# Optimization experiments

Hardware: AMD Instinct MI355X
Metric: run time of the kernel (lower is better)

The kernel has to match this reference:

```python
import jax, jax.numpy as jnp
import numpy as np


def setup_inputs() -> dict:
    key = jax.random.key(0)
    ks = jax.random.split(key, 12)
    N, E, D_IN, D_H, R, B, G, C, D_E = 50000, 600000, 128, 128, 8, 4, 64, 16, 16
    x = jax.random.normal(ks[0], (N, D_IN), dtype=jnp.float32)
    edge_index = jax.random.randint(ks[1], (2, E), 0, N, dtype=jnp.int64)
    edge_type = jax.random.randint(ks[2], (E,), 0, R, dtype=jnp.int64)
    edge_attr = jax.random.normal(ks[3], (E, D_E), dtype=jnp.float32)
    batch = jnp.sort(jax.random.randint(ks[4], (N,), 0, G, dtype=jnp.int64))
    # RGCNConv basis-decomposition params + root + bias
    basis = jax.random.normal(ks[5], (B, D_IN, D_H), dtype=jnp.float32) / np.sqrt(D_IN)
    comp = jax.random.normal(ks[6], (R, B), dtype=jnp.float32) / np.sqrt(B)
    root = jax.random.normal(ks[7], (D_IN, D_H), dtype=jnp.float32) / np.sqrt(D_IN)
    bias = jnp.zeros((D_H,), dtype=jnp.float32)
    fc_w = jax.random.normal(ks[8], (D_H, C), dtype=jnp.float32) / np.sqrt(D_H)
    fc_b = jnp.zeros((C,), dtype=jnp.float32)
    return {"x": x, "edge_index": edge_index, "edge_type": edge_type,
            "edge_attr": edge_attr, "batch": batch, "num_graphs": 64,
            "basis": basis, "comp": comp, "root": root, "bias": bias,
            "fc_w": fc_w, "fc_b": fc_b}


def reference(x, edge_index, edge_type, edge_attr, batch, num_graphs,
              basis, comp, root, bias, fc_w, fc_b):
    N = x.shape[0]
    R = comp.shape[0]
    src, dst = edge_index[0], edge_index[1]
    # relation weights from basis decomposition: [R, in, out]
    W = jnp.einsum('rb,bio->rio', comp, basis)
    x_src = x[src]  # gather source features [E, in]
    agg = jnp.zeros((N, W.shape[2]), dtype=x.dtype)
    # per-relation mean aggregation (PyG RGCNConv default), summed over relations
    for r in range(R):
        mask = (edge_type == r).astype(x.dtype)  # [E]
        msg = (x_src @ W[r]) * mask[:, None]     # [E, out]
        summed = jax.ops.segment_sum(msg, dst, num_segments=N)
        cnt = jax.ops.segment_sum(mask, dst, num_segments=N)
        agg = agg + summed / jnp.maximum(cnt, 1.0)[:, None]
    h = jax.nn.relu(x @ root + bias + agg)       # [N, hidden]
    # global mean pool over graphs
    pooled_sum = jax.ops.segment_sum(h, batch, num_segments=num_graphs)
    gcnt = jax.ops.segment_sum(jnp.ones((N,), dtype=x.dtype), batch, num_segments=num_graphs)
    pooled = pooled_sum / jnp.maximum(gcnt, 1.0)[:, None]  # [G, hidden]
    return pooled @ fc_w + fc_b                  # [G, num_classes]
```

## Files before the change

kernel.cpp:

```cpp
#include <hip/hip_runtime.h>

static inline int ceil_div(int a, int b){ return (a+b-1)/b; }
static inline size_t align_up(size_t x, size_t a){ return (x + a - 1) / a * a; }

typedef __bf16 bf16x8 __attribute__((ext_vector_type(8)));
typedef float  f32x4  __attribute__((ext_vector_type(4)));

static __device__ inline unsigned short f2bf(float f){
    unsigned int u = __float_as_uint(f);
    unsigned int lsb = (u >> 16) & 1u;
    u += 0x7FFFu + lsb;
    return (unsigned short)(u >> 16);
}
static __device__ inline float bf2f(unsigned short b){
    return __uint_as_float(((unsigned int)b) << 16);
}
static __device__ inline unsigned int packbf(float a, float b){
    return (unsigned int)f2bf(a) | ((unsigned int)f2bf(b) << 16);
}

static __device__ inline void gload_lds16(const void* g, void* l) {
    __builtin_amdgcn_global_load_lds(
        (const __attribute__((address_space(1))) unsigned int*)g,
        (__attribute__((address_space(3))) unsigned int*)l, 16, 0, 0);
}

__global__ void compute_Bt_kernel(const float* __restrict__ comp, const float* __restrict__ basis,
                                  const float* __restrict__ root, unsigned short* __restrict__ Bt,
                                  int B) {
    int idx = blockIdx.x*blockDim.x + threadIdx.x;
    if (idx >= 128*1152) return;
    int o = idx / 1152, kk = idx - o*1152;
    float val;
    if (kk < 1024) {
        int r = kk >> 7, i = kk & 127;
        val = 0.f;
        for (int b = 0; b < B; ++b)
            val += comp[r*B+b] * basis[((size_t)b*128 + i)*128 + o];
    } else {
        val = root[(size_t)(kk-1024)*128 + o];
    }
    Bt[idx] = f2bf(val);
}

__global__ void count_kernel(const int* __restrict__ dst, const int* __restrict__ et,
                             int* __restrict__ cnt, int E, int R) {
    int e = blockIdx.x*blockDim.x + threadIdx.x;
    if (e >= E) return;
    atomicAdd(&cnt[(size_t)dst[e]*R + et[e]], 1);
}

__global__ __launch_bounds__(256)
void scan_block_kernel(const int* __restrict__ in, int* __restrict__ out,
                       int* __restrict__ bsums, int n) {
    __shared__ int tsum[256];
    int t = threadIdx.x;
    int idx0 = blockIdx.x*1024 + t*4;
    int v0 = (idx0+0 < n) ? in[idx0+0] : 0;
    int v1 = (idx0+1 < n) ? in[idx0+1] : 0;
    int v2 = (idx0+2 < n) ? in[idx0+2] : 0;
    int v3 = (idx0+3 < n) ? in[idx0+3] : 0;
    int s = v0+v1+v2+v3;
    tsum[t] = s; __syncthreads();
    for (int off = 1; off < 256; off <<= 1) {
        int x = (t >= off) ? tsum[t-off] : 0;
        __syncthreads();
        tsum[t] += x;
        __syncthreads();
    }
    int run = tsum[t] - s;
    if (idx0+0 < n) out[idx0+0] = run; run += v0;
    if (idx0+1 < n) out[idx0+1] = run; run += v1;
    if (idx0+2 < n) out[idx0+2] = run; run += v2;
    if (idx0+3 < n) out[idx0+3] = run;
    if (bsums && t == 255) bsums[blockIdx.x] = tsum[255];
}

__global__ void scan_add_kernel(int* __restrict__ out, const int* __restrict__ bs,
                                int n, int total) {
    int i = blockIdx.x*blockDim.x + threadIdx.x;
    if (i < n) out[i] += bs[i >> 10];
    if (i == 0) out[n] = total;
}

__global__ void fill_kernel(const int* __restrict__ src, const int* __restrict__ dst,
                            const int* __restrict__ et, int* __restrict__ offsets,
                            int* __restrict__ slot_src, int E, int R) {
    int e = blockIdx.x*blockDim.x + threadIdx.x;
    if (e >= E) return;
    int bin = dst[e]*R + et[e];
    int slot = atomicAdd(&offsets[bin], 1);
    slot_src[slot] = src[e];
}

__global__ __launch_bounds__(256)
void xb_kernel(const float* __restrict__ x, unsigned int* __restrict__ Xb2, int N) {
    int t = blockIdx.x*blockDim.x + threadIdx.x;
    int n = t >> 6;
    if (n >= N) return;
    int l = t & 63;
    float2 v = reinterpret_cast<const float2*>(x + (size_t)n*128)[l];
    Xb2[(size_t)n*64 + l] = packbf(v.x, v.y);
}

__global__ __launch_bounds__(256)
void aggregate_kernel(const int* __restrict__ offsets, const int* __restrict__ slot_src,
                      const unsigned int* __restrict__ Xb2, unsigned int* __restrict__ Mc2,
                      int N) {
    int gw = (int)((blockIdx.x*blockDim.x + threadIdx.x) >> 6);
    int node = gw >> 2, part = gw & 3;
    if (node >= N) return;
    int l = threadIdx.x & 63;
    int base = node*8 + part*2;
    int lo   = (base == 0) ? 0 : offsets[base-1];
    int bmid = offsets[base];
    int hi   = offsets[base+1];

    float ax0=0.f, ay0=0.f, ax1=0.f, ay1=0.f;

#define ACC2(E_, U_) { \
    float vx_ = bf2f((unsigned short)((U_) & 0xFFFFu)); \
    float vy_ = bf2f((unsigned short)((U_) >> 16)); \
    if ((E_) < bmid) { ax0 += vx_; ay0 += vy_; } \
    else             { ax1 += vx_; ay1 += vy_; } }

    for (int e = lo; e < hi; e += 4) {
        int hm = hi - 1;
        int i1 = (e+1 < hm) ? e+1 : hm;
        int i2 = (e+2 < hm) ? e+2 : hm;
        int i3 = (e+3 < hm) ? e+3 : hm;
        int s0 = slot_src[e];
        int s1 = slot_src[i1];
        int s2 = slot_src[i2];
        int s3 = slot_src[i3];
        unsigned int u0 = Xb2[(size_t)s0*64 + l];
        unsigned int u1 = Xb2[(size_t)s1*64 + l];
        unsigned int u2 = Xb2[(size_t)s2*64 + l];
        unsigned int u3 = Xb2[(size_t)s3*64 + l];
        if (e+1 >= hi) u1 = 0u;
        if (e+2 >= hi) u2 = 0u;
        if (e+3 >= hi) u3 = 0u;
        ACC2(e+0, u0) ACC2(e+1, u1) ACC2(e+2, u2) ACC2(e+3, u3)
    }
#undef ACC2

    unsigned int* Mrow = Mc2 + (size_t)node*512;
    float i0 = 1.f/fmaxf((float)(bmid-lo), 1.f);
    float i1 = 1.f/fmaxf((float)(hi-bmid), 1.f);
    __builtin_nontemporal_store(packbf(ax0*i0, ay0*i0), &Mrow[(2*part+0)*64 + l]);
    __builtin_nontemporal_store(packbf(ax1*i1, ay1*i1), &Mrow[(2*part+1)*64 + l]);
}

__global__ __launch_bounds__(256)
void mfma_gemm_kernel(const unsigned short* __restrict__ Mc,
                      const unsigned short* __restrict__ Xb,
                      const unsigned short* __restrict__ Btc,
                      const float* __restrict__ bias,
                      unsigned short* __restrict__ h) {
    __shared__ char ldsA[64*128];
    __shared__ char ldsB[128*128];

    int tid  = threadIdx.x;
    int lane = tid & 63;
    int wid  = tid >> 6;
    int rg = wid & 1, cg = wid >> 1;
    int fr = lane & 15, kb = lane >> 4;
    long m0 = (long)blockIdx.x * 64;

    int lrow8 = lane >> 3;
    int lcb   = (lane & 7) * 16;

    f32x4 acc[2][4];
    #pragma unroll
    for (int mf = 0; mf < 2; ++mf)
        #pragma unroll
        for (int nf = 0; nf < 4; ++nf) acc[mf][nf] = f32x4{0.f,0.f,0.f,0.f};

    const char* McB = (const char*)Mc;
    const char* XbB = (const char*)Xb;
    const char* BtB = (const char*)Btc;

    for (int t = 0; t < 18; ++t) {
        #pragma unroll
        for (int i = 0; i < 2; ++i) {
            int row = wid*16 + i*8 + lrow8;
            int sw  = lcb ^ ((row & 7) << 4);
            const char* g = (t < 16)
                ? McB + (size_t)(m0 + row)*2048 + t*128 + sw
                : XbB + (size_t)(m0 + row)*256 + (t-16)*128 + sw;
            gload_lds16(g, &ldsA[wid*2048 + i*1024 + lane*16]);
        }
        #pragma unroll
        for (int i = 0; i < 4; ++i) {
            int col = wid*32 + i*8 + lrow8;
            int sw  = lcb ^ ((col & 7) << 4);
            const char* g = BtB + (size_t)col*2304 + t*128 + sw;
            gload_lds16(g, &ldsB[wid*4096 + i*1024 + lane*16]);
        }
        __syncthreads();

        bf16x8 af[2][2], bf[4][2];
        #pragma unroll
        for (int mf = 0; mf < 2; ++mf) {
            int row = rg*32 + mf*16 + fr;
            #pragma unroll
            for (int kk = 0; kk < 2; ++kk) {
                int byte = row*128 + ((kk*64 + kb*16) ^ ((row & 7) << 4));
                af[mf][kk] = *reinterpret_cast<const bf16x8*>(&ldsA[byte]);
            }
        }
        #pragma unroll
        for (int nf = 0; nf < 4; ++nf) {
            int col = cg*64 + nf*16 + fr;
            #pragma unroll
            for (int kk = 0; kk < 2; ++kk) {
                int byte = col*128 + ((kk*64 + kb*16) ^ ((col & 7) << 4));
                bf[nf][kk] = *reinterpret_cast<const bf16x8*>(&ldsB[byte]);
            }
        }
        #pragma unroll
        for (int kk = 0; kk < 2; ++kk)
            #pragma unroll
            for (int mf = 0; mf < 2; ++mf)
                #pragma unroll
                for (int nf = 0; nf < 4; ++nf)
                    acc[mf][nf] = __builtin_amdgcn_mfma_f32_16x16x32_bf16(
                        af[mf][kk], bf[nf][kk], acc[mf][nf], 0, 0, 0);
        __syncthreads();
    }

    float bb[4];
    #pragma unroll
    for (int nf = 0; nf < 4; ++nf) bb[nf] = bias[cg*64 + nf*16 + fr];

    #pragma unroll
    for (int mf = 0; mf < 2; ++mf)
        #pragma unroll
        for (int q = 0; q < 4; ++q) {
            long r = m0 + rg*32 + mf*16 + kb*4 + q;
            unsigned short* hr = h + (size_t)r*128 + cg*64;
            #pragma unroll
            for (int nf = 0; nf < 4; ++nf)
                hr[nf*16 + fr] = f2bf(fmaxf(acc[mf][nf][q] + bb[nf], 0.f));
        }
}

__global__ __launch_bounds__(512)
void pool_fc_kernel(const unsigned int* __restrict__ h2, const int* __restrict__ batch,
                    const float* __restrict__ fw, const float* __restrict__ fb,
                    float* __restrict__ out, int N, int C) {
    int g = blockIdx.x;
    int t = threadIdx.x;
    int lo = 0, hi = N;
    while (lo < hi) { int mid = (lo+hi) >> 1; if (batch[mid] < g) lo = mid+1; else hi = mid; }
    int s0 = lo;
    hi = N;
    while (lo < hi) { int mid = (lo+hi) >> 1; if (batch[mid] < g+1) lo = mid+1; else hi = mid; }
    int s1 = lo;

    int d2 = t & 63;
    float ax = 0.f, ay = 0.f;
    for (int row = s0 + (t >> 6); row < s1; row += 8) {
        unsigned int u = h2[(size_t)row*64 + d2];
        ax += bf2f((unsigned short)(u & 0xFFFFu));
        ay += bf2f((unsigned short)(u >> 16));
    }
    __shared__ float ps[128];
    if (t < 128) ps[t] = 0.f;
    __syncthreads();
    atomicAdd(&ps[2*d2],   ax);
    atomicAdd(&ps[2*d2+1], ay);
    __syncthreads();
    if (t < C) {
        float inv = 1.f / fmaxf((float)(s1 - s0), 1.f);
        float s = 0.f;
        #pragma unroll 4
        for (int k = 0; k < 128; ++k) s += ps[k] * fw[(size_t)k*C + t];
        out[(size_t)g*C + t] = s * inv + fb[t];
    }
}

extern "C" void kernel_launch(void* const* d_in, const int* in_sizes, int n_in,
                              void* d_out, int out_size, void* d_ws, size_t ws_size,
                              hipStream_t stream) {
    const float* x       = (const float*)d_in[0];
    const int*   eindex  = (const int*)  d_in[1];
    const int*   etype   = (const int*)  d_in[2];
    const int*   batch   = (const int*)  d_in[4];
    const float* basis   = (const float*)d_in[6];
    const float* comp    = (const float*)d_in[7];
    const float* root    = (const float*)d_in[8];
    const float* bias    = (const float*)d_in[9];
    const float* fc_w    = (const float*)d_in[10];
    const float* fc_b    = (const float*)d_in[11];

    int N  = in_sizes[4];
    int E  = in_sizes[2];
    int C  = in_sizes[11];
    int G  = out_size / C;
    int IO = in_sizes[8];
    int B  = in_sizes[6] / IO;
    int R  = in_sizes[7] / B;
    int NR = N * R;
    int MB = ceil_div(N, 64);
    int Mpad = MB * 64;

    const int* src = eindex;
    const int* dst = eindex + E;

    char* base = (char*)d_ws;
    size_t off = 0;
    auto alloc = [&](size_t bytes) -> char* {
        char* p = base + off;
        off = align_up(off + bytes, 256);
        return p;
    };
    unsigned short* Bt  = (unsigned short*)alloc(sizeof(unsigned short)*128*1152);
    int*   cnt      = (int*)  alloc(sizeof(int)*(size_t)NR);
    int*   offsets  = (int*)  alloc(sizeof(int)*((size_t)NR+1));
    int*   bsums    = (int*)  alloc(sizeof(int)*1024);
    int*   slot_src = (int*)  alloc(sizeof(int)*(size_t)E);
    unsigned short* h  = (unsigned short*)alloc(sizeof(unsigned short)*(size_t)Mpad*128);
    unsigned short* Xb = (unsigned short*)alloc(sizeof(unsigned short)*(size_t)Mpad*128);
    unsigned short* Mc = (unsigned short*)alloc(sizeof(unsigned short)*(size_t)Mpad*1024);

    hipMemsetAsync(cnt, 0, sizeof(int)*(size_t)NR, stream);
    compute_Bt_kernel<<<ceil_div(128*1152,256),256,0,stream>>>(comp, basis, root, Bt, B);
    count_kernel<<<ceil_div(E,256),256,0,stream>>>(dst, etype, cnt, E, R);

    int nb = ceil_div(NR, 1024);
    scan_block_kernel<<<nb,256,0,stream>>>(cnt, offsets, bsums, NR);
    scan_block_kernel<<<1,256,0,stream>>>(bsums, bsums, nullptr, nb);
    scan_add_kernel<<<ceil_div(NR,256),256,0,stream>>>(offsets, bsums, NR, E);

    fill_kernel<<<ceil_div(E,256),256,0,stream>>>(src, dst, etype, offsets, slot_src, E, R);

    xb_kernel<<<ceil_div(N*64,256),256,0,stream>>>(x, (unsigned int*)Xb, N);
    aggregate_kernel<<<ceil_div(N*4*64,256),256,0,stream>>>(offsets, slot_src,
                                                            (const unsigned int*)Xb,
                                                            (unsigned int*)Mc, N);

    mfma_gemm_kernel<<<MB,256,0,stream>>>(Mc, Xb, Bt, bias, h);

    pool_fc_kernel<<<G,512,0,stream>>>((const unsigned int*)h, batch, fc_w, fc_b,
                                       (float*)d_out, N, C);
}
```

Measured before the change: 220.1 us.

## Split GEMM output columns across blocks, parallelize pooling, pad edge slots

The GEMM now gives each block a 64-row by 64-column output tile, so there are twice as many blocks, ordered so that eight row blocks share each column half. This raises occupancy on the 50k-row problem. Pooling is spread over 8 chunks per graph with global float atomics into a zeroed psum buffer, and a separate small FC kernel finishes the result. The slot_src array gains four zero pad entries, which removes the clamped index math in the aggregate loop. The costs are reading each A tile twice, the extra FC launch, and atomic contention.

After: 217.4 us. About the same (-1.2%).

```diff
diff --git a/kernel.cpp b/kernel.cpp
--- a/kernel.cpp
+++ b/kernel.cpp
@@ -88,6 +88,7 @@
                             int* __restrict__ slot_src, int E, int R) {
     int e = blockIdx.x*blockDim.x + threadIdx.x;
     if (e >= E) return;
+    if (e < 4) slot_src[E + e] = 0;
     int bin = dst[e]*R + et[e];
     int slot = atomicAdd(&offsets[bin], 1);
     slot_src[slot] = src[e];
@@ -125,14 +126,10 @@
     else             { ax1 += vx_; ay1 += vy_; } }
 
     for (int e = lo; e < hi; e += 4) {
-        int hm = hi - 1;
-        int i1 = (e+1 < hm) ? e+1 : hm;
-        int i2 = (e+2 < hm) ? e+2 : hm;
-        int i3 = (e+3 < hm) ? e+3 : hm;
         int s0 = slot_src[e];
-        int s1 = slot_src[i1];
-        int s2 = slot_src[i2];
-        int s3 = slot_src[i3];
+        int s1 = slot_src[e+1];
+        int s2 = slot_src[e+2];
+        int s3 = slot_src[e+3];
         unsigned int u0 = Xb2[(size_t)s0*64 + l];
         unsigned int u1 = Xb2[(size_t)s1*64 + l];
         unsigned int u2 = Xb2[(size_t)s2*64 + l];
@@ -156,25 +153,31 @@
                       const unsigned short* __restrict__ Xb,
                       const unsigned short* __restrict__ Btc,
                       const float* __restrict__ bias,
-                      unsigned short* __restrict__ h) {
+                      unsigned short* __restrict__ h, int MBrows) {
     __shared__ char ldsA[64*128];
-    __shared__ char ldsB[128*128];
+    __shared__ char ldsB[64*128];
 
     int tid  = threadIdx.x;
     int lane = tid & 63;
     int wid  = tid >> 6;
     int rg = wid & 1, cg = wid >> 1;
     int fr = lane & 15, kb = lane >> 4;
-    long m0 = (long)blockIdx.x * 64;
+
+    int blk = blockIdx.x;
+    int q = blk >> 4, rem = blk & 15, c = rem >> 3, m = rem & 7;
+    int rb = q*8 + m;
+    if (rb >= MBrows) return;
+    long m0 = (long)rb * 64;
+    int colbase = c * 64;
 
     int lrow8 = lane >> 3;
     int lcb   = (lane & 7) * 16;
 
-    f32x4 acc[2][4];
+    f32x4 acc[2][2];
     #pragma unroll
     for (int mf = 0; mf < 2; ++mf)
         #pragma unroll
-        for (int nf = 0; nf < 4; ++nf) acc[mf][nf] = f32x4{0.f,0.f,0.f,0.f};
+        for (int nf = 0; nf < 2; ++nf) acc[mf][nf] = f32x4{0.f,0.f,0.f,0.f};
 
     const char* McB = (const char*)Mc;
     const char* XbB = (const char*)Xb;
@@ -191,15 +194,15 @@
             gload_lds16(g, &ldsA[wid*2048 + i*1024 + lane*16]);
         }
         #pragma unroll
-        for (int i = 0; i < 4; ++i) {
-            int col = wid*32 + i*8 + lrow8;
+        for (int i = 0; i < 2; ++i) {
+            int col = wid*16 + i*8 + lrow8;
             int sw  = lcb ^ ((col & 7) << 4);
-            const char* g = BtB + (size_t)col*2304 + t*128 + sw;
-            gload_lds16(g, &ldsB[wid*4096 + i*1024 + lane*16]);
+            const char* g = BtB + (size_t)(colbase + col)*2304 + t*128 + sw;
+            gload_lds16(g, &ldsB[wid*2048 + i*1024 + lane*16]);
         }
         __syncthreads();
 
-        bf16x8 af[2][2], bf[4][2];
+        bf16x8 af[2][2], bfr[2][2];
         #pragma unroll
         for (int mf = 0; mf < 2; ++mf) {
             int row = rg*32 + mf*16 + fr;
@@ -210,12 +213,12 @@
             }
         }
         #pragma unroll
-        for (int nf = 0; nf < 4; ++nf) {
-            int col = cg*64 + nf*16 + fr;
+        for (int nf = 0; nf < 2; ++nf) {
+            int col = cg*32 + nf*16 + fr;
             #pragma unroll
             for (int kk = 0; kk < 2; ++kk) {
                 int byte = col*128 + ((kk*64 + kb*16) ^ ((col & 7) << 4));
-                bf[nf][kk] = *reinterpret_cast<const bf16x8*>(&ldsB[byte]);
+                bfr[nf][kk] = *reinterpret_cast<const bf16x8*>(&ldsB[byte]);
             }
         }
         #pragma unroll
@@ -223,32 +226,31 @@
             #pragma unroll
             for (int mf = 0; mf < 2; ++mf)
                 #pragma unroll
-                for (int nf = 0; nf < 4; ++nf)
+                for (int nf = 0; nf < 2; ++nf)
                     acc[mf][nf] = __builtin_amdgcn_mfma_f32_16x16x32_bf16(
-                        af[mf][kk], bf[nf][kk], acc[mf][nf], 0, 0, 0);
+                        af[mf][kk], bfr[nf][kk], acc[mf][nf], 0, 0, 0);
         __syncthreads();
     }
 
-    float bb[4];
+    float bb[2];
     #pragma unroll
-    for (int nf = 0; nf < 4; ++nf) bb[nf] = bias[cg*64 + nf*16 + fr];
+    for (int nf = 0; nf < 2; ++nf) bb[nf] = bias[colbase + cg*32 + nf*16 + fr];
 
     #pragma unroll
     for (int mf = 0; mf < 2; ++mf)
         #pragma unroll
-        for (int q = 0; q < 4; ++q) {
-            long r = m0 + rg*32 + mf*16 + kb*4 + q;
-            unsigned short* hr = h + (size_t)r*128 + cg*64;
+        for (int q2 = 0; q2 < 4; ++q2) {
+            long r = m0 + rg*32 + mf*16 + kb*4 + q2;
+            unsigned short* hr = h + (size_t)r*128 + colbase + cg*32;
             #pragma unroll
-            for (int nf = 0; nf < 4; ++nf)
-                hr[nf*16 + fr] = f2bf(fmaxf(acc[mf][nf][q] + bb[nf], 0.f));
-        }
-}
-
-__global__ __launch_bounds__(512)
-void pool_fc_kernel(const unsigned int* __restrict__ h2, const int* __restrict__ batch,
-                    const float* __restrict__ fw, const float* __restrict__ fb,
-                    float* __restrict__ out, int N, int C) {
+            for (int nf = 0; nf < 2; ++nf)
+                hr[nf*16 + fr] = f2bf(fmaxf(acc[mf][nf][q2] + bb[nf], 0.f));
+        }
+}
+
+__global__ __launch_bounds__(256)
+void pool_kernel(const unsigned int* __restrict__ h2, const int* __restrict__ batch,
+                 float* __restrict__ psum, int N) {
     int g = blockIdx.x;
     int t = threadIdx.x;
     int lo = 0, hi = N;
@@ -257,27 +259,39 @@
     hi = N;
     while (lo < hi) { int mid = (lo+hi) >> 1; if (batch[mid] < g+1) lo = mid+1; else hi = mid; }
     int s1 = lo;
+    int len = s1 - s0;
+    int chunk = blockIdx.y, NC = gridDim.y;
+    int a = s0 + (int)((long long)len * chunk / NC);
+    int b = s0 + (int)((long long)len * (chunk+1) / NC);
 
     int d2 = t & 63;
     float ax = 0.f, ay = 0.f;
-    for (int row = s0 + (t >> 6); row < s1; row += 8) {
+    for (int row = a + (t >> 6); row < b; row += 4) {
         unsigned int u = h2[(size_t)row*64 + d2];
         ax += bf2f((unsigned short)(u & 0xFFFFu));
         ay += bf2f((unsigned short)(u >> 16));
     }
-    __shared__ float ps[128];
-    if (t < 128) ps[t] = 0.f;
-    __syncthreads();
-    atomicAdd(&ps[2*d2],   ax);
-    atomicAdd(&ps[2*d2+1], ay);
-    __syncthreads();
-    if (t < C) {
-        float inv = 1.f / fmaxf((float)(s1 - s0), 1.f);
-        float s = 0.f;
-        #pragma unroll 4
-        for (int k = 0; k < 128; ++k) s += ps[k] * fw[(size_t)k*C + t];
-        out[(size_t)g*C + t] = s * inv + fb[t];
-    }
+    atomicAdd(&psum[(size_t)g*128 + 2*d2    ], ax);
+    atomicAdd(&psum[(size_t)g*128 + 2*d2 + 1], ay);
+}
+
+__global__ void fc_kernel(const float* __restrict__ psum, const int* __restrict__ batch,
+                          const float* __restrict__ fw, const float* __restrict__ fb,
+                          float* __restrict__ out, int N, int G, int C) {
+    int idx = blockIdx.x*blockDim.x + threadIdx.x;
+    if (idx >= G*C) return;
+    int g = idx / C, cc = idx - g*C;
+    int lo = 0, hi = N;
+    while (lo < hi) { int mid = (lo+hi) >> 1; if (batch[mid] < g) lo = mid+1; else hi = mid; }
+    int s0 = lo;
+    hi = N;
+    while (lo < hi) { int mid = (lo+hi) >> 1; if (batch[mid] < g+1) lo = mid+1; else hi = mid; }
+    float inv = 1.f / fmaxf((float)(lo - s0), 1.f);
+    float s = fb[cc];
+    #pragma unroll 4
+    for (int k = 0; k < 128; ++k)
+        s += psum[(size_t)g*128 + k] * inv * fw[(size_t)k*C + cc];
+    out[idx] = s;
 }
 
 extern "C" void kernel_launch(void* const* d_in, const int* in_sizes, int n_in,
@@ -304,6 +318,7 @@
     int NR = N * R;
     int MB = ceil_div(N, 64);
     int Mpad = MB * 64;
+    int grid_gemm = ceil_div(MB, 8) * 16;
 
     const int* src = eindex;
     const int* dst = eindex + E;
@@ -317,14 +332,15 @@
     };
     unsigned short* Bt  = (unsigned short*)alloc(sizeof(unsigned short)*128*1152);
     int*   cnt      = (int*)  alloc(sizeof(int)*(size_t)NR);
+    float* psum     = (float*)alloc(sizeof(float)*(size_t)G*128);
     int*   offsets  = (int*)  alloc(sizeof(int)*((size_t)NR+1));
     int*   bsums    = (int*)  alloc(sizeof(int)*1024);
-    int*   slot_src = (int*)  alloc(sizeof(int)*(size_t)E);
+    int*   slot_src = (int*)  alloc(sizeof(int)*((size_t)E+4));
     unsigned short* h  = (unsigned short*)alloc(sizeof(unsigned short)*(size_t)Mpad*128);
     unsigned short* Xb = (unsigned short*)alloc(sizeof(unsigned short)*(size_t)Mpad*128);
     unsigned short* Mc = (unsigned short*)alloc(sizeof(unsigned short)*(size_t)Mpad*1024);
 
-    hipMemsetAsync(cnt, 0, sizeof(int)*(size_t)NR, stream);
+    hipMemsetAsync(cnt, 0, (size_t)((char*)(psum + (size_t)G*128) - (char*)cnt), stream);
     compute_Bt_kernel<<<ceil_div(128*1152,256),256,0,stream>>>(comp, basis, root, Bt, B);
     count_kernel<<<ceil_div(E,256),256,0,stream>>>(dst, etype, cnt, E, R);
 
@@ -340,8 +356,9 @@
                                                             (const unsigned int*)Xb,
                                                             (unsigned int*)Mc, N);
 
-    mfma_gemm_kernel<<<MB,256,0,stream>>>(Mc, Xb, Bt, bias, h);
-
-    pool_fc_kernel<<<G,512,0,stream>>>((const unsigned int*)h, batch, fc_w, fc_b,
-                                       (float*)d_out, N, C);
-}
+    mfma_gemm_kernel<<<grid_gemm,256,0,stream>>>(Mc, Xb, Bt, bias, h, MB);
+
+    pool_kernel<<<dim3(G,8),256,0,stream>>>((const unsigned int*)h, batch, psum, N);
+    fc_kernel<<<ceil_div(G*C,256),256,0,stream>>>(psum, batch, fc_w, fc_b,
+                                                  (float*)d_out, N, G, C);
+}
```
